# Kernel optimization log

Hardware: AMD Instinct MI355X
Metric: run time of the kernel (lower is better)

## Reference

```python
import jax, jax.numpy as jnp
import numpy as np

N = 384          # residues / nodes
E = 12288        # edges (avg degree 32)
D_LM = 1024      # BERT hidden
D_NODE = 256     # extra node features -> D_LM + D_NODE = 1280
D = 1280         # node_emb_size
H = D // 10      # 128, dis/mask MLP hidden
M = 64           # masked positions


def setup_inputs() -> dict:
    key = jax.random.key(0)
    ks = jax.random.split(key, 16)
    s = lambda d_in: 1.0 / np.sqrt(d_in)
    inp = {
        "lm_embedding": jax.random.normal(ks[0], (1, N + 2, D_LM), jnp.float32),
        "node_feat": jax.random.normal(ks[1], (N, D_NODE), jnp.float32),
        # positive distances in [0.5, 1.5) so edge_weight = 1/(d^2+1e-6) is well scaled
        "edge_feat": jax.random.uniform(ks[2], (E, 1), jnp.float32) + 0.5,
        "src": jax.random.randint(ks[3], (E,), 0, N, jnp.int32),
        "dst": jax.random.randint(ks[4], (E,), 0, N, jnp.int32),
        "mask_index": jax.random.randint(ks[5], (M,), 0, N, jnp.int32),
        # GINConv apply-func linears (stored as [in, out]; torch Linear is x @ W.T + b)
        "W_gin0": jax.random.normal(ks[6], (D, D), jnp.float32) * s(D),
        "b_gin0": jnp.zeros((D,), jnp.float32),
        "W_gin1": jax.random.normal(ks[7], (D, D), jnp.float32) * s(D),
        "b_gin1": jnp.zeros((D,), jnp.float32),
        # dis_nn: Linear(D,H) -> ReLU -> Linear(H,30)
        "Wd1": jax.random.normal(ks[8], (D, H), jnp.float32) * s(D),
        "bd1": jnp.zeros((H,), jnp.float32),
        "Wd2": jax.random.normal(ks[9], (H, 30), jnp.float32) * s(H),
        "bd2": jnp.zeros((30,), jnp.float32),
        # mask_nn: Linear(D,H) -> ReLU -> Linear(H,2) -> Tanh
        "Wm1": jax.random.normal(ks[10], (D, H), jnp.float32) * s(D),
        "bm1": jnp.zeros((H,), jnp.float32),
        "Wm2": jax.random.normal(ks[11], (H, 2), jnp.float32) * s(H),
        "bm2": jnp.zeros((2,), jnp.float32),
    }
    return inp


def _gin(x, src, dst, edge_weight, W, b):
    # DGL GINConv (eps=0, 'sum'): Linear( x + sum_{e:(u->v)} w_e * x_u )
    msg = x[src] * edge_weight                      # [E, D] gather-multiply
    agg = jax.ops.segment_sum(msg, dst, num_segments=N)  # scatter-sum to dst
    return (x + agg) @ W + b


def reference(lm_embedding, node_feat, edge_feat, src, dst, mask_index,
              W_gin0, b_gin0, W_gin1, b_gin1,
              Wd1, bd1, Wd2, bd2, Wm1, bm1, Wm2, bm2):
    # node_feat0: strip CLS/SEP tokens, concat with node features -> [N, D]
    node_feat0 = jnp.concatenate([lm_embedding[0, 1:-1, :], node_feat], axis=1)
    edge_weight = 1.0 / (edge_feat ** 2 + 1e-6)     # [E, 1]

    # original uses node_feat0.data (detached) as GIN input
    x0 = jax.lax.stop_gradient(node_feat0)
    h = _gin(x0, src, dst, edge_weight, W_gin0, b_gin0)
    node_output = _gin(h, src, dst, edge_weight, W_gin1, b_gin1)
    node_output = node_output + node_feat0          # residual (use_lm=1)

    # pairwise squared differences: [N, N, D]
    dis_hid = (node_output[None, :, :] - node_output[:, None, :]) ** 2
    dh = dis_hid.reshape(-1, D)                     # [N*N, D]
    dis_pred = jax.nn.relu(dh @ Wd1 + bd1) @ Wd2 + bd2  # [N*N, 30]

    xm = node_output[mask_index]                    # [M, D]
    mask_pred = jnp.tanh(jax.nn.relu(xm @ Wm1 + bm1) @ Wm2 + bm2)  # [M, 2]
    return dis_pred, mask_pred
```

## Files before the change

### kernel.cpp

```cpp
#include <hip/hip_runtime.h>
#include <hip/hip_bf16.h>

#define NN 384
#define EE 12288
#define DD 1280
#define HH 128
#define DISROWS (NN*NN)

typedef short bf16x8 __attribute__((ext_vector_type(8)));
typedef short bf16x4 __attribute__((ext_vector_type(4)));
typedef float f32x4  __attribute__((ext_vector_type(4)));

__device__ __forceinline__ unsigned short f2bf(float x){
  unsigned u = __builtin_bit_cast(unsigned, x);
  u += 0x7fffu + ((u >> 16) & 1u);
  return (unsigned short)(u >> 16);
}
__device__ __forceinline__ float bf2f(unsigned short h){
  unsigned u = ((unsigned)h) << 16;
  return __builtin_bit_cast(float, u);
}
__device__ __forceinline__ short f2bf_fast(float x){
  return (short)__bfloat16_as_ushort(__float2bfloat16(x));
}
__device__ __forceinline__ void glds16(const short* g, short* l){
  __builtin_amdgcn_global_load_lds((const __attribute__((address_space(1))) void*)g,
                                   (__attribute__((address_space(3))) void*)l, 16, 0, 0);
}

__device__ __forceinline__ void tsplit_body(const float* __restrict__ W,
                                            short* __restrict__ Thi, short* __restrict__ Tlo,
                                            int R, int C, int bx, int by, int t,
                                            float* tile ){
  int rb = by*64, cb = bx*64;
  int r  = t >> 2;
  int cs = (t & 3) * 16;
  const float* sp = W + (long)(rb + r)*C + cb + cs;
  #pragma unroll
  for (int i = 0; i < 16; i += 4){
    f32x4 v = *(const f32x4*)(sp + i);
    tile[r*65 + cs+i+0] = v[0]; tile[r*65 + cs+i+1] = v[1];
    tile[r*65 + cs+i+2] = v[2]; tile[r*65 + cs+i+3] = v[3];
  }
  __syncthreads();
  int cp = t >> 2;
  int rs = (t & 3) * 16;
  bf16x8 vh0, vh1, vl0, vl1;
  #pragma unroll
  for (int i = 0; i < 8; ++i){
    float f = tile[(rs+i)*65 + cp];
    unsigned short h = f2bf(f);
    vh0[i] = (short)h; vl0[i] = (short)f2bf(f - bf2f(h));
  }
  #pragma unroll
  for (int i = 0; i < 8; ++i){
    float f = tile[(rs+8+i)*65 + cp];
    unsigned short h = f2bf(f);
    vh1[i] = (short)h; vl1[i] = (short)f2bf(f - bf2f(h));
  }
  long ob = (long)(cb + cp)*R + rb + rs;
  *(bf16x8*)&Thi[ob]   = vh0;
  *(bf16x8*)&Thi[ob+8] = vh1;
  if (Tlo){
    *(bf16x8*)&Tlo[ob]   = vl0;
    *(bf16x8*)&Tlo[ob+8] = vl1;
  }
}

__global__ void k_prep(const float* __restrict__ lm, const float* __restrict__ nf,
                       float* __restrict__ x0,
                       const int* __restrict__ dst, const float* __restrict__ ef,
                       int* __restrict__ offs, int* __restrict__ sorted,
                       float* __restrict__ ew,
                       const float* __restrict__ Wd1, short* __restrict__ W1t,
                       const float* __restrict__ Wd2, short* __restrict__ W2t,
                       const float* __restrict__ Wg0, short* __restrict__ WtAh,
                       short* __restrict__ WtAl){
  __shared__ __align__(16) float sh[64*65];
  const int b = blockIdx.x;
  const int t = threadIdx.x;
  if (b < 960){
    int i = b*512 + t;
    int n = i / 1280;
    int d = i - n*1280;
    x0[i] = (d < 1024) ? lm[(n+1)*1024 + d] : nf[n*256 + (d-1024)];
    return;
  }
  if (b == 960){
    int* cnt = (int*)sh;
    int* base = cnt + 512;
    if (t < 512) cnt[t] = 0;
    __syncthreads();
    for (int e = t; e < EE; e += 512){
      atomicAdd(&cnt[dst[e]], 1);
      float f = ef[e];
      ew[e] = 1.0f/(f*f + 1e-6f);
    }
    __syncthreads();
    for (int off = 1; off < 512; off <<= 1){
      int v = (t >= off) ? cnt[t - off] : 0;
      __syncthreads();
      cnt[t] += v;
      __syncthreads();
    }
    if (t < NN){
      int excl = t ? cnt[t-1] : 0;
      offs[t] = excl;
      base[t] = excl;
    }
    if (t == 0) offs[NN] = EE;
    __syncthreads();
    for (int e = t; e < EE; e += 512){
      int p = atomicAdd(&base[dst[e]], 1);
      sorted[p] = e;
    }
    return;
  }
  if (b < 1002){
    int g = b - 961;
    if (g < 40){
      if (t < 256) tsplit_body(Wd1, W1t, nullptr, DD, HH, g & 1, g >> 1, t, sh);
      else { __syncthreads(); }
      return;
    }
    for (int i = t; i < 32*HH; i += 512){
      int c = i >> 7, h = i & 127;
      float v = (c < 30) ? Wd2[h*30 + c] : 0.f;
      W2t[i] = (short)f2bf(v);
    }
    return;
  }
  {
    int g = b - 1002;
    if (t < 256) tsplit_body(Wg0, WtAh, WtAl, DD, DD, g % 20, g / 20, t, sh);
    else { __syncthreads(); }
  }
}

__global__ void k_agg(const float* __restrict__ X, const float* __restrict__ ew,
                      const int* __restrict__ src, const int* __restrict__ offs,
                      const int* __restrict__ sorted,
                      short* __restrict__ Yh, short* __restrict__ Yl){
  __shared__ int   s_off[160];
  __shared__ float s_w[160];
  const int v = blockIdx.x;
  const int d = blockIdx.y*256 + threadIdx.x;
  const int t = threadIdx.x;
  float acc = X[(long)v*DD + d];
  const int b = offs[v], e = offs[v+1];
  for (int c0 = b; c0 < e; c0 += 160){
    int n = e - c0; if (n > 160) n = 160;
    __syncthreads();
    if (t < n){
      int eid = sorted[c0 + t];
      s_off[t] = src[eid]*DD;
      s_w[t]   = ew[eid];
    }
    __syncthreads();
    int k = 0;
    for (; k + 4 <= n; k += 4){
      acc += s_w[k]  *X[s_off[k]   + d];
      acc += s_w[k+1]*X[s_off[k+1] + d];
      acc += s_w[k+2]*X[s_off[k+2] + d];
      acc += s_w[k+3]*X[s_off[k+3] + d];
    }
    for (; k < n; ++k) acc += s_w[k]*X[s_off[k] + d];
  }
  unsigned short h = f2bf(acc);
  Yh[(long)v*DD + d] = (short)h;
  Yl[(long)v*DD + d] = (short)f2bf(acc - bf2f(h));
}

__launch_bounds__(256, 2)
__global__ void k_gin_gemm(const short* __restrict__ Yh, const short* __restrict__ Yl,
                           const short* __restrict__ Whi, const short* __restrict__ Wlo,
                           float* __restrict__ P){
  __shared__ __align__(16) short Ahi[128*40], Alo[128*40], Bhi[128*40], Blo[128*40];
  const int m0 = blockIdx.x*128;
  const int n0 = blockIdx.y*128;
  const int kbase = blockIdx.z*160;
  const int t = threadIdx.x, w = t >> 6, lane = t & 63;
  const int l15 = lane & 15, l4 = lane >> 4;
  f32x4 acc[2][8];
  #pragma unroll
  for (int m = 0; m < 2; ++m)
    #pragma unroll
    for (int n = 0; n < 8; ++n) acc[m][n] = (f32x4){0.f,0.f,0.f,0.f};

  const int row = t >> 1, half = t & 1;
  const short* aph = Yh  + (long)(m0+row)*DD + half*16;
  const short* apl = Yl  + (long)(m0+row)*DD + half*16;
  const short* bph = Whi + (long)(n0+row)*DD + half*16;
  const short* bpl = Wlo + (long)(n0+row)*DD + half*16;

  for (int kk = 0; kk < 5; ++kk){
    int d0 = kbase + kk*32;
    __syncthreads();
    *(bf16x8*)&Ahi[row*40 + half*16]     = *(const bf16x8*)(aph + d0);
    *(bf16x8*)&Ahi[row*40 + half*16 + 8] = *(const bf16x8*)(aph + d0 + 8);
    *(bf16x8*)&Alo[row*40 + half*16]     = *(const bf16x8*)(apl + d0);
    *(bf16x8*)&Alo[row*40 + half*16 + 8] = *(const bf16x8*)(apl + d0 + 8);
    *(bf16x8*)&Bhi[row*40 + half*16]     = *(const bf16x8*)(bph + d0);
    *(bf16x8*)&Bhi[row*40 + half*16 + 8] = *(const bf16x8*)(bph + d0 + 8);
    *(bf16x8*)&Blo[row*40 + half*16]     = *(const bf16x8*)(bpl + d0);
    *(bf16x8*)&Blo[row*40 + half*16 + 8] = *(const bf16x8*)(bpl + d0 + 8);
    __syncthreads();

    bf16x8 ah[2], al[2];
    #pragma unroll
    for (int m = 0; m < 2; ++m){
      int rr = w*32 + m*16 + l15;
      ah[m] = *(const bf16x8*)&Ahi[rr*40 + l4*8];
      al[m] = *(const bf16x8*)&Alo[rr*40 + l4*8];
    }
    #pragma unroll
    for (int n = 0; n < 8; ++n){
      int rr = n*16 + l15;
      bf16x8 bh = *(const bf16x8*)&Bhi[rr*40 + l4*8];
      bf16x8 bl = *(const bf16x8*)&Blo[rr*40 + l4*8];
      #pragma unroll
      for (int m = 0; m < 2; ++m){
        acc[m][n] = __builtin_amdgcn_mfma_f32_16x16x32_bf16(ah[m], bh, acc[m][n], 0,0,0);
        acc[m][n] = __builtin_amdgcn_mfma_f32_16x16x32_bf16(ah[m], bl, acc[m][n], 0,0,0);
        acc[m][n] = __builtin_amdgcn_mfma_f32_16x16x32_bf16(al[m], bh, acc[m][n], 0,0,0);
      }
    }
  }
  float* Pz = P + (long)blockIdx.z*NN*DD;
  #pragma unroll
  for (int m = 0; m < 2; ++m){
    #pragma unroll
    for (int n = 0; n < 8; ++n){
      int gr0 = m0 + w*32 + m*16 + l4*4;
      int gc  = n0 + n*16 + l15;
      #pragma unroll
      for (int r = 0; r < 4; ++r)
        Pz[(long)(gr0+r)*DD + gc] = acc[m][n][r];
    }
  }
}

__global__ void k_red_t(const float* __restrict__ P, const float* __restrict__ bias,
                        const float* __restrict__ resid, float* __restrict__ Out,
                        const float* __restrict__ Wg1, short* __restrict__ WtAh,
                        short* __restrict__ WtAl){
  __shared__ __align__(16) float sh[64*65];
  const int b = blockIdx.x;
  if (b >= 480){
    if (Wg1){
      int g = b - 480;
      tsplit_body(Wg1, WtAh, WtAl, DD, DD, g % 20, g / 20, threadIdx.x, sh);
    }
    return;
  }
  const int i = b*256 + threadIdx.x;
  const int col = (i*4) % DD;
  const f32x4* P4 = (const f32x4*)P;
  f32x4 s = P4[i];
  #pragma unroll
  for (int z = 1; z < 8; ++z) s += P4[i + z*122880];
  s += *(const f32x4*)(bias + col);
  if (resid) s += ((const f32x4*)resid)[i];
  ((f32x4*)Out)[i] = s;
}

__launch_bounds__(512, 4)
__global__ void k_dis(const float* __restrict__ X, const short* __restrict__ W1t,
                      const float* __restrict__ bd1, const short* __restrict__ W2t,
                      const float* __restrict__ bd2, float* __restrict__ out,
                      const int* __restrict__ midx,
                      const float* __restrict__ Wm1, const float* __restrict__ bm1,
                      const float* __restrict__ Wm2, const float* __restrict__ bm2){
  __shared__ __align__(16) short smem[25088];
  const int b = blockIdx.x;
  const int t = threadIdx.x;

  if (b >= 600){
    float* tl = (float*)smem;
    int m = b - 600;
    if (t < HH){
      const float* x = X + (long)midx[m]*DD;
      float a0 = 0.f, a1 = 0.f, a2 = 0.f, a3 = 0.f;
      for (int d = 0; d < DD; d += 4){
        a0 += x[d]   * Wm1[(d)*HH + t];
        a1 += x[d+1] * Wm1[(d+1)*HH + t];
        a2 += x[d+2] * Wm1[(d+2)*HH + t];
        a3 += x[d+3] * Wm1[(d+3)*HH + t];
      }
      float v = a0 + a1 + a2 + a3 + bm1[t];
      tl[t] = v > 0.f ? v : 0.f;
    }
    __syncthreads();
    if (t < 2){
      float s = bm2[t];
      for (int h = 0; h < HH; ++h) s += tl[h]*Wm2[h*2 + t];
      out[(long)DISROWS*30 + m*2 + t] = tanhf(s);
    }
    return;
  }

  int k = 0, rem = b;
  while (rem >= 2*(24 - k)){ rem -= 2*(24 - k); ++k; }
  int ib = 2*k;
  if (rem >= 24 - k){ ++ib; rem -= 24 - k; }
  const int jb = k + rem;
  const int i0 = ib*8, j0 = jb*16;

  const int w = t >> 6, lane = t & 63;
  const int l15 = lane & 15, l4 = lane >> 4;

  short* WA = smem;
  float* XF = (float*)(smem + 16384);
  short* TL = smem;
  float* OT = (float*)(smem + 17408);

  f32x4 acc[8];
  #pragma unroll
  for (int n = 0; n < 8; ++n) acc[n] = (f32x4){0.f,0.f,0.f,0.f};

  const short* wsrc[2];
  #pragma unroll
  for (int i = 0; i < 2; ++i){
    int hb = w*16 + i*8 + (lane >> 3);
    wsrc[i] = W1t + (long)hb*DD + (((lane & 7) ^ (hb & 7))*8);
  }
  const float* xsrc[3];
  int xli[3];
  #pragma unroll
  for (int g = 0; g < 3; ++g){
    int idx = g*512 + t;
    int rowl = idx >> 6, col = idx & 63;
    int grow = (rowl < 8) ? (i0 + rowl) : (j0 + rowl - 8);
    xsrc[g] = X + (long)grow*DD + col;
    xli[g] = rowl*68 + col;
  }

  float xr[3];
  glds16(wsrc[0], WA + (w*16)*64);
  glds16(wsrc[1], WA + (w*16 + 8)*64);
  #pragma unroll
  for (int g = 0; g < 3; ++g) xr[g] = xsrc[g][0];
  #pragma unroll
  for (int g = 0; g < 3; ++g) XF[xli[g]] = xr[g];
  __syncthreads();

  for (int mk = 0; mk < 20; ++mk){
    const int cb = mk & 1;
    short* WAc = WA + cb*8192;
    float* XFc = XF + cb*1632;
    short* WAn = WA + (cb^1)*8192;
    float* XFn = XF + (cb^1)*1632;
    if (mk < 19){
      glds16(wsrc[0] + (mk+1)*64, WAn + (w*16)*64);
      glds16(wsrc[1] + (mk+1)*64, WAn + (w*16 + 8)*64);
      #pragma unroll
      for (int g = 0; g < 3; ++g) xr[g] = xsrc[g][(mk+1)*64];
    }
    #pragma unroll
    for (int ks = 0; ks < 2; ++ks){
      f32x4 xj0 = *(const f32x4*)&XFc[(8 + l15)*68 + ks*32 + l4*8];
      f32x4 xj1 = *(const f32x4*)&XFc[(8 + l15)*68 + ks*32 + l4*8 + 4];
      const float* xip = &XFc[w*68 + ks*32 + l4*8];
      f32x4 xi0 = *(const f32x4*)xip;
      f32x4 xi1 = *(const f32x4*)(xip + 4);
      f32x4 d0 = xj0 - xi0; d0 = d0*d0;
      f32x4 d1 = xj1 - xi1; d1 = d1*d1;
      bf16x8 a;
      #pragma unroll
      for (int q = 0; q < 4; ++q){
        a[q]   = f2bf_fast(d0[q]);
        a[4+q] = f2bf_fast(d1[q]);
      }
      #pragma unroll
      for (int n = 0; n < 8; ++n){
        bf16x8 wf = *(const bf16x8*)&WAc[(n*16 + l15)*64 + (((ks*4 + l4) ^ (l15 & 7))*8)];
        acc[n] = __builtin_amdgcn_mfma_f32_16x16x32_bf16(wf, a, acc[n], 0,0,0);
      }
    }
    if (mk < 19){
      #pragma unroll
      for (int g = 0; g < 3; ++g) XFn[xli[g]] = xr[g];
    }
    __syncthreads();
  }

  f32x4 bd1v[8];
  #pragma unroll
  for (int n = 0; n < 8; ++n) bd1v[n] = *(const f32x4*)(bd1 + n*16 + l4*4);
  {
    int pair = w*16 + l15;
    #pragma unroll
    for (int n = 0; n < 8; ++n){
      bf16x4 pv;
      #pragma unroll
      for (int r = 0; r < 4; ++r){
        float v = acc[n][r] + bd1v[n][r];
        v = v > 0.f ? v : 0.f;
        pv[r] = f2bf_fast(v);
      }
      *(bf16x4*)&TL[pair*136 + n*16 + l4*4] = pv;
    }
  }
  __syncthreads();

  f32x4 acc2[2];
  acc2[0] = (f32x4){0.f,0.f,0.f,0.f};
  acc2[1] = (f32x4){0.f,0.f,0.f,0.f};
  #pragma unroll
  for (int hs = 0; hs < 4; ++hs){
    bf16x8 a2 = *(const bf16x8*)&TL[(w*16 + l15)*136 + hs*32 + l4*8];
    #pragma unroll
    for (int nn = 0; nn < 2; ++nn){
      bf16x8 b2 = *(const bf16x8*)&W2t[(nn*16 + l15)*HH + hs*32 + l4*8];
      acc2[nn] = __builtin_amdgcn_mfma_f32_16x16x32_bf16(a2, b2, acc2[nn], 0,0,0);
    }
  }
  #pragma unroll
  for (int nn = 0; nn < 2; ++nn){
    int cc = nn*16 + l15;
    if (cc < 30){
      float b2v = bd2[cc];
      #pragma unroll
      for (int r = 0; r < 4; ++r)
        OT[(w*16 + l4*4 + r)*30 + cc] = acc2[nn][r] + b2v;
    }
  }
  __syncthreads();

  if (t < 256){
    int i = t >> 5;
    int ca = (t & 31)*15;
    long nbase = ((long)(i0 + i)*NN + j0)*30 + ca;
    const float* nsrc = OT + i*480 + ca;
    #pragma unroll
    for (int q = 0; q < 15; ++q) out[nbase + q] = nsrc[q];
  } else {
    int tt = t - 256;
    int j = tt >> 4;
    int s = tt & 15;
    int ii = s >> 1;
    int c0 = (s & 1)*15;
    long mbase = ((long)(j0 + j)*NN + i0 + ii)*30 + c0;
    const float* msrc = OT + ii*480 + j*30 + c0;
    #pragma unroll
    for (int q = 0; q < 15; ++q) out[mbase + q] = msrc[q];
  }
}

extern "C" void kernel_launch(void* const* d_in, const int* in_sizes, int n_in,
                              void* d_out, int out_size, void* d_ws, size_t ws_size,
                              hipStream_t stream){
  const float* lm   = (const float*)d_in[0];
  const float* nf   = (const float*)d_in[1];
  const float* ef   = (const float*)d_in[2];
  const int*   src  = (const int*)d_in[3];
  const int*   dst  = (const int*)d_in[4];
  const int*   midx = (const int*)d_in[5];
  const float* Wg0  = (const float*)d_in[6];
  const float* bg0  = (const float*)d_in[7];
  const float* Wg1  = (const float*)d_in[8];
  const float* bg1  = (const float*)d_in[9];
  const float* Wd1  = (const float*)d_in[10];
  const float* bd1  = (const float*)d_in[11];
  const float* Wd2  = (const float*)d_in[12];
  const float* bd2  = (const float*)d_in[13];
  const float* Wm1  = (const float*)d_in[14];
  const float* bm1  = (const float*)d_in[15];
  const float* Wm2  = (const float*)d_in[16];
  const float* bm2  = (const float*)d_in[17];
  float* dis = (float*)d_out;

  char* ws = (char*)d_ws;
  size_t off = 0;
  auto alloc = [&](size_t bytes)->void*{
    void* p = ws + off; off += (bytes + 255) & ~(size_t)255; return p;
  };
  float* x0   = (float*)alloc((size_t)NN*DD*4);
  float* hb   = (float*)alloc((size_t)NN*DD*4);
  short* Yh   = (short*)alloc((size_t)NN*DD*2);
  short* Yl   = (short*)alloc((size_t)NN*DD*2);
  float* ew   = (float*)alloc((size_t)EE*4);
  int*   offs = (int*)alloc((NN+1)*4);
  int*   sorted = (int*)alloc(EE*4);
  short* WtAh = (short*)alloc((size_t)DD*DD*2);
  short* WtAl = (short*)alloc((size_t)DD*DD*2);
  short* W1t  = (short*)alloc((size_t)HH*DD*2);
  short* W2t  = (short*)alloc((size_t)32*HH*2);
  float* P    = (float*)alloc((size_t)8*NN*DD*4);

  k_prep<<<1402,512,0,stream>>>(lm, nf, x0, dst, ef, offs, sorted, ew,
                                Wd1, W1t, Wd2, W2t, Wg0, WtAh, WtAl);

  k_agg<<<dim3(384,5),256,0,stream>>>(x0, ew, src, offs, sorted, Yh, Yl);
  k_gin_gemm<<<dim3(3,10,8),256,0,stream>>>(Yh, Yl, WtAh, WtAl, P);
  k_red_t<<<880,256,0,stream>>>(P, bg0, nullptr, hb, Wg1, WtAh, WtAl);

  k_agg<<<dim3(384,5),256,0,stream>>>(hb, ew, src, offs, sorted, Yh, Yl);
  k_gin_gemm<<<dim3(3,10,8),256,0,stream>>>(Yh, Yl, WtAh, WtAl, P);
  k_red_t<<<480,256,0,stream>>>(P, bg1, x0, hb, nullptr, nullptr, nullptr);

  k_dis<<<664,512,0,stream>>>(hb, W1t, bd1, W2t, bd2, dis,
                              midx, Wm1, bm1, Wm2, bm2);
}
```

Before: 135.9 us.

## Split K across two warp groups in dis MLP and reduce partials through LDS

The eight warps of the distance-MLP block are split into two groups, each handling half of the 1280-wide reduction dimension with its own smaller double-buffered W and X tiles. Each warp now computes two i-rows at once, so every loaded W fragment feeds two MFMAs. After the main loop, group 1 writes its partial accumulators to shared memory and group 0 adds them before the bias/ReLU and second layer. This aims to cut LDS fragment reads per MFMA and shorten the per-block K loop. In exchange it doubles accumulator registers, adds an LDS reduction with extra barriers, and leaves half the warps idle in the epilogue.

```diff
diff --git a/kernel.cpp b/kernel.cpp
--- a/kernel.cpp
+++ b/kernel.cpp
@@ -308,97 +308,132 @@
 
   const int w = t >> 6, lane = t & 63;
   const int l15 = lane & 15, l4 = lane >> 4;
-
-  short* WA = smem;
-  float* XF = (float*)(smem + 16384);
+  const int g = w >> 2, wa = w & 3;
+  const int tl256 = t & 255;
+
+  short* WG = smem + g*8192;
+  float* XG = (float*)(smem + 16384) + g*1728;
+  float* HB = (float*)smem;
   short* TL = smem;
   float* OT = (float*)(smem + 17408);
 
-  f32x4 acc[8];
-  #pragma unroll
-  for (int n = 0; n < 8; ++n) acc[n] = (f32x4){0.f,0.f,0.f,0.f};
-
-  const short* wsrc[2];
+  f32x4 acc[2][8];
+  #pragma unroll
+  for (int m = 0; m < 2; ++m)
+    #pragma unroll
+    for (int n = 0; n < 8; ++n) acc[m][n] = (f32x4){0.f,0.f,0.f,0.f};
+
+  const short* wsrc[2]; int wdst[2];
   #pragma unroll
   for (int i = 0; i < 2; ++i){
-    int hb = w*16 + i*8 + (lane >> 3);
-    wsrc[i] = W1t + (long)hb*DD + (((lane & 7) ^ (hb & 7))*8);
+    int hb = wa*32 + i*16 + (lane >> 2);
+    wsrc[i] = W1t + (long)hb*DD + g*640 + (((lane & 3) ^ ((hb >> 1) & 3))*8);
+    wdst[i] = (wa*32 + i*16)*32;
   }
   const float* xsrc[3];
   int xli[3];
   #pragma unroll
-  for (int g = 0; g < 3; ++g){
-    int idx = g*512 + t;
-    int rowl = idx >> 6, col = idx & 63;
+  for (int q = 0; q < 3; ++q){
+    int idx = q*256 + tl256;
+    int rowl = idx >> 5, col = idx & 31;
     int grow = (rowl < 8) ? (i0 + rowl) : (j0 + rowl - 8);
-    xsrc[g] = X + (long)grow*DD + col;
-    xli[g] = rowl*68 + col;
+    xsrc[q] = X + (long)grow*DD + g*640 + col;
+    xli[q] = rowl*36 + col;
   }
 
   float xr[3];
-  glds16(wsrc[0], WA + (w*16)*64);
-  glds16(wsrc[1], WA + (w*16 + 8)*64);
-  #pragma unroll
-  for (int g = 0; g < 3; ++g) xr[g] = xsrc[g][0];
-  #pragma unroll
-  for (int g = 0; g < 3; ++g) XF[xli[g]] = xr[g];
+  glds16(wsrc[0], WG + wdst[0]);
+  glds16(wsrc[1], WG + wdst[1]);
+  #pragma unroll
+  for (int q = 0; q < 3; ++q) xr[q] = xsrc[q][0];
+  #pragma unroll
+  for (int q = 0; q < 3; ++q) XG[xli[q]] = xr[q];
   __syncthreads();
 
+  const int wro = (l4 ^ ((l15 >> 1) & 3))*8;
   for (int mk = 0; mk < 20; ++mk){
     const int cb = mk & 1;
-    short* WAc = WA + cb*8192;
-    float* XFc = XF + cb*1632;
-    short* WAn = WA + (cb^1)*8192;
-    float* XFn = XF + (cb^1)*1632;
+    short* WAc = WG + cb*4096;
+    float* XFc = XG + cb*864;
     if (mk < 19){
-      glds16(wsrc[0] + (mk+1)*64, WAn + (w*16)*64);
-      glds16(wsrc[1] + (mk+1)*64, WAn + (w*16 + 8)*64);
-      #pragma unroll
-      for (int g = 0; g < 3; ++g) xr[g] = xsrc[g][(mk+1)*64];
-    }
-    #pragma unroll
-    for (int ks = 0; ks < 2; ++ks){
-      f32x4 xj0 = *(const f32x4*)&XFc[(8 + l15)*68 + ks*32 + l4*8];
-      f32x4 xj1 = *(const f32x4*)&XFc[(8 + l15)*68 + ks*32 + l4*8 + 4];
-      const float* xip = &XFc[w*68 + ks*32 + l4*8];
+      glds16(wsrc[0] + (mk+1)*32, WG + (cb^1)*4096 + wdst[0]);
+      glds16(wsrc[1] + (mk+1)*32, WG + (cb^1)*4096 + wdst[1]);
+      #pragma unroll
+      for (int q = 0; q < 3; ++q) xr[q] = xsrc[q][(mk+1)*32];
+    }
+    f32x4 xj0 = *(const f32x4*)&XFc[(8 + l15)*36 + l4*8];
+    f32x4 xj1 = *(const f32x4*)&XFc[(8 + l15)*36 + l4*8 + 4];
+    bf16x8 a[2];
+    #pragma unroll
+    for (int m = 0; m < 2; ++m){
+      const float* xip = &XFc[(2*wa + m)*36 + l4*8];
       f32x4 xi0 = *(const f32x4*)xip;
       f32x4 xi1 = *(const f32x4*)(xip + 4);
       f32x4 d0 = xj0 - xi0; d0 = d0*d0;
       f32x4 d1 = xj1 - xi1; d1 = d1*d1;
-      bf16x8 a;
+      bf16x8 av;
       #pragma unroll
       for (int q = 0; q < 4; ++q){
-        a[q]   = f2bf_fast(d0[q]);
-        a[4+q] = f2bf_fast(d1[q]);
+        av[q]   = f2bf_fast(d0[q]);
+        av[4+q] = f2bf_fast(d1[q]);
       }
+      a[m] = av;
+    }
+    #pragma unroll
+    for (int n = 0; n < 8; ++n){
+      bf16x8 wf = *(const bf16x8*)&WAc[(n*16 + l15)*32 + wro];
+      acc[0][n] = __builtin_amdgcn_mfma_f32_16x16x32_bf16(wf, a[0], acc[0][n], 0,0,0);
+      acc[1][n] = __builtin_amdgcn_mfma_f32_16x16x32_bf16(wf, a[1], acc[1][n], 0,0,0);
+    }
+    if (mk < 19){
+      #pragma unroll
+      for (int q = 0; q < 3; ++q) XG[(cb^1)*864 + xli[q]] = xr[q];
+    }
+    __syncthreads();
+  }
+
+  #pragma unroll
+  for (int half = 0; half < 2; ++half){
+    if (g == 1){
+      #pragma unroll
+      for (int m = 0; m < 2; ++m){
+        int pr = (2*wa + m)*16 + l15;
+        #pragma unroll
+        for (int n2 = 0; n2 < 4; ++n2)
+          *(f32x4*)&HB[pr*68 + n2*16 + l4*4] = acc[m][half*4 + n2];
+      }
+    }
+    __syncthreads();
+    if (g == 0){
+      #pragma unroll
+      for (int m = 0; m < 2; ++m){
+        int pr = (2*wa + m)*16 + l15;
+        #pragma unroll
+        for (int n2 = 0; n2 < 4; ++n2)
+          acc[m][half*4 + n2] += *(const f32x4*)&HB[pr*68 + n2*16 + l4*4];
+      }
+    }
+    __syncthreads();
+  }
+
+  if (g == 0){
+    f32x4 bd1v[8];
+    #pragma unroll
+    for (int n = 0; n < 8; ++n) bd1v[n] = *(const f32x4*)(bd1 + n*16 + l4*4);
+    #pragma unroll
+    for (int m = 0; m < 2; ++m){
+      int pair = (2*wa + m)*16 + l15;
       #pragma unroll
       for (int n = 0; n < 8; ++n){
-        bf16x8 wf = *(const bf16x8*)&WAc[(n*16 + l15)*64 + (((ks*4 + l4) ^ (l15 & 7))*8)];
-        acc[n] = __builtin_amdgcn_mfma_f32_16x16x32_bf16(wf, a, acc[n], 0,0,0);
+        bf16x4 pv;
+        #pragma unroll
+        for (int r = 0; r < 4; ++r){
+          float v = acc[m][n][r] + bd1v[n][r];
+          v = v > 0.f ? v : 0.f;
+          pv[r] = f2bf_fast(v);
+        }
+        *(bf16x4*)&TL[pair*136 + n*16 + l4*4] = pv;
       }
-    }
-    if (mk < 19){
-      #pragma unroll
-      for (int g = 0; g < 3; ++g) XFn[xli[g]] = xr[g];
-    }
-    __syncthreads();
-  }
-
-  f32x4 bd1v[8];
-  #pragma unroll
-  for (int n = 0; n < 8; ++n) bd1v[n] = *(const f32x4*)(bd1 + n*16 + l4*4);
-  {
-    int pair = w*16 + l15;
-    #pragma unroll
-    for (int n = 0; n < 8; ++n){
-      bf16x4 pv;
-      #pragma unroll
-      for (int r = 0; r < 4; ++r){
-        float v = acc[n][r] + bd1v[n][r];
-        v = v > 0.f ? v : 0.f;
-        pv[r] = f2bf_fast(v);
-      }
-      *(bf16x4*)&TL[pair*136 + n*16 + l4*4] = pv;
     }
   }
   __syncthreads();
```

Measured after the change: 138.5 us. No clear change (+1.9%).
